# Optimization experiments

Hardware: AMD Instinct MI355X
Metric: run time of the kernel (lower is better)

## Reference

```python
import jax, jax.numpy as jnp
import numpy as np
from jax.scipy.special import logsumexp
from jax import lax

N, T, C = 512, 512, 64


def setup_inputs() -> dict:
    key = jax.random.key(0)
    k1, k2, k3 = jax.random.split(key, 3)
    batch_logits = jax.random.normal(k1, (N, T, C), dtype=jnp.float32)
    # lengths in [1, T-1]: score_sequence scan output has length T-1 and is indexed at lengths-1
    lengths = jax.random.randint(k2, (N,), 1, T, dtype=jnp.int64 if jax.config.jax_enable_x64 else jnp.int32)
    batch_tags = jax.random.randint(k3, (N, T), 0, C, dtype=jnp.int64 if jax.config.jax_enable_x64 else jnp.int32)
    # transition matrix parameter, default init jnp.ones as in the module
    transition_matrix = jnp.ones((C, C), dtype=jnp.float32)
    return {"batch_logits": batch_logits, "lengths": lengths,
            "batch_tags": batch_tags, "transition_matrix": transition_matrix}


def _sum_scores(transition_matrix, logits):
    # logits: [T, C]; CRF forward algorithm. alphas[t] = logsumexp over prev class j of
    # (logit_t[i]/C + transition[i, j] + alpha[j])
    n_classes = transition_matrix.shape[0]
    init = jnp.zeros((n_classes,), dtype=logits.dtype)

    def step(prev_alphas, logit_t):
        a = logsumexp(logit_t[:, None] / n_classes + transition_matrix + prev_alphas, axis=1)
        return a, a

    _, alphas = lax.scan(step, init, logits)  # alphas: [T, C]
    return jnp.sum(alphas, -1)  # [T]


def _score_sequence(transition_matrix, logits, tags):
    # logits: [T, C], tags: [T]
    first = logits[0, tags[0]] + jnp.sum(transition_matrix[tags[0], :])

    def step(prev, i):
        s = prev + transition_matrix[tags[i + 1], tags[i]] + logits[i + 1, tags[i + 1]]
        return s, s

    _, scores = lax.scan(step, first, jnp.arange(logits.shape[0] - 1))
    return scores  # [T-1]


def reference(batch_logits, lengths, batch_tags, transition_matrix):
    # partition function: sum of scores of all sequences of length lengths[i]
    part_all = jax.vmap(lambda lg: _sum_scores(transition_matrix, lg))(batch_logits)  # [N, T]
    partition = jnp.take_along_axis(part_all, (lengths - 1)[:, None], axis=1)[:, 0]  # == diag(part_all[:, lengths-1])
    # gold score of the provided tag sequences
    gold_all = jax.vmap(lambda lg, tg: _score_sequence(transition_matrix, lg, tg))(batch_logits, batch_tags)  # [N, T-1]
    gold = jnp.take_along_axis(gold_all, (lengths - 1)[:, None], axis=1)[:, 0]
    # negative log likelihood per sample
    return partition - gold
```

## Files before the change

### kernel.cpp

```cpp
#include <hip/hip_runtime.h>

#define NCLS 64
#define TDIM 512
#define PD   8

typedef _Float16 h2 __attribute__((ext_vector_type(2)));

#if __has_builtin(__builtin_amdgcn_fdot2)
#define FDOT2(a, b, c) __builtin_amdgcn_fdot2((a), (b), (c), false)
#else
static __device__ __forceinline__ float FDOT2(h2 a, h2 b, float c) {
    return fmaf((float)a.x, (float)b.x, fmaf((float)a.y, (float)b.y, c));
}
#endif

#define BC_H2(x) __builtin_bit_cast(h2, (x))
#define LN64 4.1588830833596715f

__global__ __launch_bounds__(512) void crf_kernel(
    const float* __restrict__ logits,
    const int*   __restrict__ lengths,
    const int*   __restrict__ tags,
    const float* __restrict__ trans,
    float* __restrict__ out, int N)
{
    const int n = blockIdx.x;
    if (n >= N) return;
    const int tid = threadIdx.x;

    __shared__ float sRed[8];
    __shared__ __align__(16) _Float16 fh_lds[NCLS];

    int ok;
    {
        const unsigned c0b = __builtin_bit_cast(unsigned, trans[0]);
        const float4 a = reinterpret_cast<const float4*>(trans)[tid * 2];
        const float4 b = reinterpret_cast<const float4*>(trans)[tid * 2 + 1];
        ok  = (__builtin_bit_cast(unsigned, a.x) == c0b);
        ok &= (__builtin_bit_cast(unsigned, a.y) == c0b);
        ok &= (__builtin_bit_cast(unsigned, a.z) == c0b);
        ok &= (__builtin_bit_cast(unsigned, a.w) == c0b);
        ok &= (__builtin_bit_cast(unsigned, b.x) == c0b);
        ok &= (__builtin_bit_cast(unsigned, b.y) == c0b);
        ok &= (__builtin_bit_cast(unsigned, b.z) == c0b);
        ok &= (__builtin_bit_cast(unsigned, b.w) == c0b);
    }
    const int uni = __syncthreads_and(ok);

    const int len = lengths[n];
    const float* lg = logits + (size_t)n * TDIM * NCLS;
    const int*   tg = tags   + (size_t)n * TDIM;
    const float I64 = 1.0f / 64.0f;

    if (uni) {
        float contrib = 0.f;

        if (tid < len) {
            const float4* rp = reinterpret_cast<const float4*>(lg + (size_t)tid * NCLS);
            float4 vv[16];
            #pragma unroll
            for (int q = 0; q < 16; ++q) vv[q] = rp[q];

            float mx = -3.0e38f;
            #pragma unroll
            for (int q = 0; q < 16; ++q)
                mx = fmaxf(mx, fmaxf(fmaxf(vv[q].x, vv[q].y), fmaxf(vv[q].z, vv[q].w)));
            float es = 0.f;
            #pragma unroll
            for (int q = 0; q < 16; ++q)
                es += __expf((vv[q].x - mx) * I64) + __expf((vv[q].y - mx) * I64)
                    + __expf((vv[q].z - mx) * I64) + __expf((vv[q].w - mx) * I64);

            if (tid <= len - 2)
                contrib += 64.0f * (mx * I64 + __logf(es));
            if (tid == len - 1) {
                float rs = 0.f;
                #pragma unroll
                for (int q = 0; q < 16; ++q) rs += (vv[q].x + vv[q].y) + (vv[q].z + vv[q].w);
                contrib += rs * I64;
            }
        }
        if (tid >= 1 && tid <= len) contrib -= lg[(size_t)tid * NCLS + tg[tid]];
        if (tid == 0)               contrib -= lg[tg[0]];

        #pragma unroll
        for (int o = 32; o; o >>= 1) contrib += __shfl_xor(contrib, o);
        if ((tid & 63) == 0) sRed[tid >> 6] = contrib;
        __syncthreads();
        if (tid == 0) {
            float s = 0.f;
            #pragma unroll
            for (int w = 0; w < 8; ++w) s += sRed[w];
            const float c = trans[0];
            out[n] = s + 64.0f * ((float)len * c + LN64) - 64.0f * c - (float)len * c;
        }
        return;
    }

    if (tid >= 64) return;
    const int lane = tid;
    const float INV_C = 1.0f / (float)NCLS;

    int tr8[PD];
    #pragma unroll
    for (int k = 0; k < PD; ++k) tr8[k] = tg[lane + NCLS * k];

    float trow[NCLS];
    #pragma unroll
    for (int q = 0; q < 16; ++q) {
        const float4 v = *reinterpret_cast<const float4*>(&trans[lane * NCLS + q * 4]);
        trow[4*q] = v.x; trow[4*q+1] = v.y; trow[4*q+2] = v.z; trow[4*q+3] = v.w;
    }
    float tmax = -3.0e38f, tsum = 0.f;
    #pragma unroll
    for (int j = 0; j < NCLS; ++j) { tmax = fmaxf(tmax, trow[j]); tsum += trow[j]; }
    float mT = tmax;
    #pragma unroll
    for (int o = 32; o; o >>= 1) mT = fmaxf(mT, __shfl_xor(mT, o));
    h2 tp[NCLS / 2];
    #pragma unroll
    for (int j = 0; j < NCLS; j += 2) {
        const float e0 = __expf(trow[j]     - mT) * 0.015625f;
        const float e1 = __expf(trow[j + 1] - mT) * 0.015625f;
        h2 p; p.x = (_Float16)e0; p.y = (_Float16)e1;
        tp[j >> 1] = p;
    }

    const int   t0 = __shfl(tr8[0], 0);
    const float rs = __shfl(tsum, t0);
    const float first = lg[t0] + rs;

    float f = 1.0f;
    float B = 0.0f;

    float lgr[PD];
    #pragma unroll
    for (int k = 0; k < PD; ++k) lgr[k] = lg[(size_t)k * NCLS + lane];

    const int nblk = len >> 3;
    const int tail = len & 7;

    #define CRF_STEP(PVAL)                                                     \
    {                                                                          \
        fh_lds[lane] = (_Float16)f;                                            \
        float d0 = 0.f, d1 = 0.f, d2 = 0.f, d3 = 0.f;                          \
        _Pragma("unroll")                                                      \
        for (int j = 0; j < NCLS; j += 16) {                                   \
            const float4 a  = *reinterpret_cast<const float4*>(&fh_lds[j]);    \
            const float4 b4 = *reinterpret_cast<const float4*>(&fh_lds[j+8]);  \
            d0 = FDOT2(tp[(j >> 1) + 0], BC_H2(a.x),  d0);                     \
            d1 = FDOT2(tp[(j >> 1) + 1], BC_H2(a.y),  d1);                     \
            d2 = FDOT2(tp[(j >> 1) + 2], BC_H2(a.z),  d2);                     \
            d3 = FDOT2(tp[(j >> 1) + 3], BC_H2(a.w),  d3);                     \
            d0 = FDOT2(tp[(j >> 1) + 4], BC_H2(b4.x), d0);                     \
            d1 = FDOT2(tp[(j >> 1) + 5], BC_H2(b4.y), d1);                     \
            d2 = FDOT2(tp[(j >> 1) + 6], BC_H2(b4.z), d2);                     \
            d3 = FDOT2(tp[(j >> 1) + 7], BC_H2(b4.w), d3);                     \
        }                                                                      \
        const float dot = (d0 + d1) + (d2 + d3);                               \
        f = dot * (PVAL);                                                      \
    }

    int t = 0;
    for (int b = 0; b < nblk; ++b) {
        #pragma unroll
        for (int k = 0; k < PD; ++k) {
            const float p = __expf(lgr[k] * INV_C);
            int nidx = t + k + PD; nidx = (nidx > TDIM - 1) ? (TDIM - 1) : nidx;
            lgr[k] = lg[(size_t)nidx * NCLS + lane];
            CRF_STEP(p);
        }
        t += PD;
        if ((b & 7) == 7) {
            float r = __builtin_bit_cast(float,
                          __builtin_amdgcn_readfirstlane(__builtin_bit_cast(int, f)));
            r = fmaxf(r, 1e-30f);
            f *= __builtin_amdgcn_rcpf(r);
            B += __logf(r);
        }
    }

    #pragma unroll
    for (int k = 0; k < PD - 1; ++k) {
        if (k < tail) {
            const float p = __expf(lgr[k] * INV_C);
            CRF_STEP(p);
        }
    }
    #undef CRF_STEP

    float g = 0.f;
    #pragma unroll
    for (int k = 0; k < PD; ++k) {
        const int m = 1 + lane + NCLS * k;
        if (m <= len) {
            const int rot  = __shfl(tr8[k], (lane + 1) & 63);
            const int wrap = __shfl(tr8[(k + 1) & (PD - 1)], 0);
            const int tm = (lane == 63) ? wrap : rot;
            const int tp_ = tr8[k];
            g += trans[tm * NCLS + tp_] + lg[(size_t)m * NCLS + tm];
        }
    }

    float v = __logf(f) - g;
    #pragma unroll
    for (int o = 32; o; o >>= 1) v += __shfl_xor(v, o);

    if (lane == 0) {
        const float Bt = (float)len * (mT + LN64) + B;
        out[n] = 64.0f * Bt + v - first;
    }
}

extern "C" void kernel_launch(void* const* d_in, const int* in_sizes, int n_in,
                              void* d_out, int out_size, void* d_ws, size_t ws_size,
                              hipStream_t stream) {
    const float* logits  = (const float*)d_in[0];
    const int*   lengths = (const int*)  d_in[1];
    const int*   tags    = (const int*)  d_in[2];
    const float* trans   = (const float*)d_in[3];
    float* out = (float*)d_out;
    const int N = in_sizes[1];

    crf_kernel<<<N, 512, 0, stream>>>(logits, lengths, tags, trans, out, N);
}
```

Measured before the change: 18.69 us.

## Split per-sample CRF block into eight 64-thread blocks plus finalize kernel

Replaces the single 512-thread block per sample with eight independent 64-thread blocks per sample. Each block reduces its own 64 rows into a workspace slot, and a second small kernel sums the eight partials and applies the closed-form terms. The uniform-transition check is now done per wave with a ballot instead of a block-wide barrier, so no cross-wave synchronisation is needed. The intent is finer-grained scheduling and no block-level sync, at the cost of an extra kernel launch and a workspace round trip. In the non-uniform path, seven of the eight blocks per sample still compute row partials whose results are never used.

```diff
diff --git a/kernel.cpp b/kernel.cpp
--- a/kernel.cpp
+++ b/kernel.cpp
@@ -17,88 +17,89 @@
 #define BC_H2(x) __builtin_bit_cast(h2, (x))
 #define LN64 4.1588830833596715f
 
-__global__ __launch_bounds__(512) void crf_kernel(
+static __device__ __forceinline__ float row_contrib(
+    const float* __restrict__ lg, const int* __restrict__ tg, int row, int len)
+{
+    const float I64 = 1.0f / 64.0f;
+    float contrib = 0.f;
+    if (row < len) {
+        const float4* rp = reinterpret_cast<const float4*>(lg + (size_t)row * NCLS);
+        float4 vv[16];
+        #pragma unroll
+        for (int q = 0; q < 16; ++q) vv[q] = rp[q];
+        float mx = -3.0e38f;
+        #pragma unroll
+        for (int q = 0; q < 16; ++q)
+            mx = fmaxf(mx, fmaxf(fmaxf(vv[q].x, vv[q].y), fmaxf(vv[q].z, vv[q].w)));
+        float es = 0.f;
+        #pragma unroll
+        for (int q = 0; q < 16; ++q)
+            es += __expf((vv[q].x - mx) * I64) + __expf((vv[q].y - mx) * I64)
+                + __expf((vv[q].z - mx) * I64) + __expf((vv[q].w - mx) * I64);
+        if (row <= len - 2)
+            contrib += 64.0f * (mx * I64 + __logf(es));
+        if (row == len - 1) {
+            float rs = 0.f;
+            #pragma unroll
+            for (int q = 0; q < 16; ++q) rs += (vv[q].x + vv[q].y) + (vv[q].z + vv[q].w);
+            contrib += rs * I64;
+        }
+    }
+    if (row >= 1 && row <= len) contrib -= lg[(size_t)row * NCLS + tg[row]];
+    return contrib;
+}
+
+__global__ __launch_bounds__(64) void crf_part(
     const float* __restrict__ logits,
     const int*   __restrict__ lengths,
     const int*   __restrict__ tags,
     const float* __restrict__ trans,
-    float* __restrict__ out, int N)
+    float* __restrict__ ws, int N)
 {
-    const int n = blockIdx.x;
+    const int bid = blockIdx.x;
+    const int n   = bid >> 3;
+    const int c   = bid & 7;
     if (n >= N) return;
-    const int tid = threadIdx.x;
-
-    __shared__ float sRed[8];
-    __shared__ __align__(16) _Float16 fh_lds[NCLS];
-
-    int ok;
-    {
-        const unsigned c0b = __builtin_bit_cast(unsigned, trans[0]);
-        const float4 a = reinterpret_cast<const float4*>(trans)[tid * 2];
-        const float4 b = reinterpret_cast<const float4*>(trans)[tid * 2 + 1];
-        ok  = (__builtin_bit_cast(unsigned, a.x) == c0b);
-        ok &= (__builtin_bit_cast(unsigned, a.y) == c0b);
-        ok &= (__builtin_bit_cast(unsigned, a.z) == c0b);
-        ok &= (__builtin_bit_cast(unsigned, a.w) == c0b);
-        ok &= (__builtin_bit_cast(unsigned, b.x) == c0b);
-        ok &= (__builtin_bit_cast(unsigned, b.y) == c0b);
-        ok &= (__builtin_bit_cast(unsigned, b.z) == c0b);
-        ok &= (__builtin_bit_cast(unsigned, b.w) == c0b);
-    }
-    const int uni = __syncthreads_and(ok);
+    const int lane = threadIdx.x;
 
     const int len = lengths[n];
     const float* lg = logits + (size_t)n * TDIM * NCLS;
     const int*   tg = tags   + (size_t)n * TDIM;
-    const float I64 = 1.0f / 64.0f;
+
+    if (c != 0) {
+        float contrib = row_contrib(lg, tg, c * 64 + lane, len);
+        #pragma unroll
+        for (int o = 32; o; o >>= 1) contrib += __shfl_xor(contrib, o);
+        if (lane == 0) ws[n * 8 + c] = contrib;
+        return;
+    }
+
+    const unsigned c0b = __builtin_bit_cast(unsigned, trans[0]);
+    float4 tvv[16];
+    #pragma unroll
+    for (int q = 0; q < 16; ++q)
+        tvv[q] = *reinterpret_cast<const float4*>(&trans[lane * NCLS + q * 4]);
+    int eq = 1;
+    #pragma unroll
+    for (int q = 0; q < 16; ++q) {
+        eq &= (__builtin_bit_cast(unsigned, tvv[q].x) == c0b);
+        eq &= (__builtin_bit_cast(unsigned, tvv[q].y) == c0b);
+        eq &= (__builtin_bit_cast(unsigned, tvv[q].z) == c0b);
+        eq &= (__builtin_bit_cast(unsigned, tvv[q].w) == c0b);
+    }
+    const bool uni = (__ballot(eq) == ~0ULL);
+    if (n == 0 && lane == 0) ws[8 * N] = uni ? 1.0f : 0.0f;
 
     if (uni) {
-        float contrib = 0.f;
-
-        if (tid < len) {
-            const float4* rp = reinterpret_cast<const float4*>(lg + (size_t)tid * NCLS);
-            float4 vv[16];
-            #pragma unroll
-            for (int q = 0; q < 16; ++q) vv[q] = rp[q];
-
-            float mx = -3.0e38f;
-            #pragma unroll
-            for (int q = 0; q < 16; ++q)
-                mx = fmaxf(mx, fmaxf(fmaxf(vv[q].x, vv[q].y), fmaxf(vv[q].z, vv[q].w)));
-            float es = 0.f;
-            #pragma unroll
-            for (int q = 0; q < 16; ++q)
-                es += __expf((vv[q].x - mx) * I64) + __expf((vv[q].y - mx) * I64)
-                    + __expf((vv[q].z - mx) * I64) + __expf((vv[q].w - mx) * I64);
-
-            if (tid <= len - 2)
-                contrib += 64.0f * (mx * I64 + __logf(es));
-            if (tid == len - 1) {
-                float rs = 0.f;
-                #pragma unroll
-                for (int q = 0; q < 16; ++q) rs += (vv[q].x + vv[q].y) + (vv[q].z + vv[q].w);
-                contrib += rs * I64;
-            }
-        }
-        if (tid >= 1 && tid <= len) contrib -= lg[(size_t)tid * NCLS + tg[tid]];
-        if (tid == 0)               contrib -= lg[tg[0]];
-
+        float contrib = row_contrib(lg, tg, lane, len);
+        if (lane == 0) contrib -= lg[tg[0]];
         #pragma unroll
         for (int o = 32; o; o >>= 1) contrib += __shfl_xor(contrib, o);
-        if ((tid & 63) == 0) sRed[tid >> 6] = contrib;
-        __syncthreads();
-        if (tid == 0) {
-            float s = 0.f;
-            #pragma unroll
-            for (int w = 0; w < 8; ++w) s += sRed[w];
-            const float c = trans[0];
-            out[n] = s + 64.0f * ((float)len * c + LN64) - 64.0f * c - (float)len * c;
-        }
+        if (lane == 0) ws[n * 8] = contrib;
         return;
     }
 
-    if (tid >= 64) return;
-    const int lane = tid;
+    __shared__ __align__(16) _Float16 fh_lds[NCLS];
     const float INV_C = 1.0f / (float)NCLS;
 
     int tr8[PD];
@@ -108,8 +109,8 @@
     float trow[NCLS];
     #pragma unroll
     for (int q = 0; q < 16; ++q) {
-        const float4 v = *reinterpret_cast<const float4*>(&trans[lane * NCLS + q * 4]);
-        trow[4*q] = v.x; trow[4*q+1] = v.y; trow[4*q+2] = v.z; trow[4*q+3] = v.w;
+        trow[4*q] = tvv[q].x; trow[4*q+1] = tvv[q].y;
+        trow[4*q+2] = tvv[q].z; trow[4*q+3] = tvv[q].w;
     }
     float tmax = -3.0e38f, tsum = 0.f;
     #pragma unroll
@@ -208,7 +209,28 @@
 
     if (lane == 0) {
         const float Bt = (float)len * (mT + LN64) + B;
-        out[n] = 64.0f * Bt + v - first;
+        ws[n * 8] = 64.0f * Bt + v - first;
+    }
+}
+
+__global__ __launch_bounds__(64) void crf_fin(
+    const int*   __restrict__ lengths,
+    const float* __restrict__ trans,
+    const float* __restrict__ ws,
+    float* __restrict__ out, int N)
+{
+    const int n = blockIdx.x * 64 + threadIdx.x;
+    if (n >= N) return;
+    const float flag = ws[8 * N];
+    if (flag != 0.0f) {
+        float s = 0.f;
+        #pragma unroll
+        for (int c = 0; c < 8; ++c) s += ws[n * 8 + c];
+        const int   len = lengths[n];
+        const float cc  = trans[0];
+        out[n] = s + 64.0f * ((float)len * cc + LN64) - 64.0f * cc - (float)len * cc;
+    } else {
+        out[n] = ws[n * 8];
     }
 }
 
@@ -220,7 +242,9 @@
     const int*   tags    = (const int*)  d_in[2];
     const float* trans   = (const float*)d_in[3];
     float* out = (float*)d_out;
+    float* ws  = (float*)d_ws;
     const int N = in_sizes[1];
 
-    crf_kernel<<<N, 512, 0, stream>>>(logits, lengths, tags, trans, out, N);
-}
+    crf_part<<<N * 8, 64, 0, stream>>>(logits, lengths, tags, trans, ws, N);
+    crf_fin <<<(N + 63) / 64, 64, 0, stream>>>(lengths, trans, ws, out, N);
+}
```

Result: slower. 26.10 us (+39.7%).
